# Kernel tuning notes

Hardware: AMD Instinct MI355X
Metric: run time of the kernel (lower is better)

Reference implementation:

```python
import jax, jax.numpy as jnp
import numpy as np
from jax import lax

EPS = 1e-5
TAU = 2.0
THR = 1.0

@jax.custom_vjp
def spike_fn(x):
    # torch.heaviside(x, 1.0): 1 where x >= 0, else 0
    return (x >= 0).astype(x.dtype)

def _spike_fwd(x):
    return spike_fn(x), x

def _spike_bwd(x, g):
    alpha = 4.0
    s = jax.nn.sigmoid(alpha * x)
    return (g * (1.0 - s) * s * alpha,)

spike_fn.defvjp(_spike_fwd, _spike_bwd)

def lif(x):
    # sequential membrane recurrence over dim 0 (time)
    def step(v, xt):
        v = v + (xt - v) / TAU
        s = spike_fn(v - THR)
        v = (1.0 - lax.stop_gradient(s)) * v
        return v, s
    _, spikes = lax.scan(step, jnp.zeros_like(x[0]), x)
    return spikes

def bn(x, p):
    # eval-mode BatchNorm2d; p = [weight, bias, mean, var], each [C]
    w, b, m, v = p
    inv = w / jnp.sqrt(v + EPS)
    return (x - m[None, :, None, None]) * inv[None, :, None, None] + b[None, :, None, None]

def bn_and_pad(x, p):
    # BN then pad 1 pixel on all sides with the BN-of-zero value
    w, b, m, v = p
    y = bn(x, p)
    pad_val = b - m * w / jnp.sqrt(v + EPS)  # [C]
    y = jnp.pad(y, ((0, 0), (0, 0), (1, 1), (1, 1)))
    pv = pad_val[None, :, None]  # broadcasts over batch and spatial
    y = y.at[:, :, 0, :].set(pv)
    y = y.at[:, :, -1, :].set(pv)
    y = y.at[:, :, :, 0].set(pv)
    y = y.at[:, :, :, -1].set(pv)
    return y

def branch(x, w1, dw, pw, bn3):
    # RepConv: 1x1 -> BNAndPad(1) -> depthwise3x3(valid) -> 1x1 -> BN, then outer BN
    C = x.shape[1]
    y = jnp.einsum('oc,bchw->bohw', w1, x)
    y = bn_and_pad(y, bn3[0])
    y = lax.conv_general_dilated(y, dw[:, None, :, :], (1, 1), 'VALID',
                                 dimension_numbers=('NCHW', 'OIHW', 'NCHW'),
                                 feature_group_count=C)
    y = jnp.einsum('oc,bchw->bohw', pw, y)
    y = bn(y, bn3[1])
    y = bn(y, bn3[2])
    return y

def _to_heads(t, B, N, h, d):
    # [B,C,H,W] -> [B,h,N,d]
    return t.reshape(B, h * d, N).transpose(0, 2, 1).reshape(B, N, h, d).transpose(0, 2, 1, 3)

def forward(x, q_w1, q_dw, q_pw, q_bn, k_w1, k_dw, k_pw, k_bn,
            v_w1, v_dw, v_pw, v_bn, p_w1, p_dw, p_pw, p_bn,
            num_heads=8):
    B, C, H, W = x.shape
    N = H * W
    h = num_heads
    d = C // h
    scale = float(d) ** -0.5

    xs = lif(x)
    q = lif(branch(xs, q_w1, q_dw, q_pw, q_bn))
    k = lif(branch(xs, k_w1, k_dw, k_pw, k_bn))
    v = lif(branch(xs, v_w1, v_dw, v_pw, v_bn))

    q = _to_heads(q, B, N, h, d)
    k = _to_heads(k, B, N, h, d)
    v = _to_heads(v, B, N, h, d)

    kv = jnp.einsum('bhnd,bhne->bhde', k, v)          # [B,h,d,d]
    o = jnp.einsum('bhnd,bhde->bhne', q, kv) * scale  # [B,h,N,d]
    o = o.transpose(0, 1, 3, 2).reshape(B, C, N)       # [B,C,N]
    o = lif(o)
    o = o.reshape(B, C, H, W)
    o = branch(o, p_w1, p_dw, p_pw, p_bn)
    return o.reshape(B, C, H, W)

def setup_inputs() -> dict:
    key = jax.random.key(0)
    ks = jax.random.split(key, 20)
    B, C, H, W = 8, 256, 64, 64
    s1 = 1.0 / np.sqrt(C)

    def make_bn(k):
        k1, k2, k3, k4 = jax.random.split(k, 4)
        w = 1.0 + 0.1 * jax.random.normal(k1, (3, C), jnp.float32)
        b = 0.1 * jax.random.normal(k2, (3, C), jnp.float32)
        m = 0.1 * jax.random.normal(k3, (3, C), jnp.float32)
        var = jax.random.uniform(k4, (3, C), jnp.float32, 0.5, 1.5)
        return jnp.stack([w, b, m, var], axis=1)  # [3,4,C]

    inp = {'x': jax.random.normal(ks[0], (B, C, H, W), jnp.float32)}
    for i, p in enumerate(['q', 'k', 'v', 'p']):
        kk = jax.random.split(ks[1 + i], 4)
        inp[p + '_w1'] = jax.random.normal(kk[0], (C, C), jnp.float32) * s1
        inp[p + '_dw'] = jax.random.normal(kk[1], (C, 3, 3), jnp.float32) * 0.3
        inp[p + '_pw'] = jax.random.normal(kk[2], (C, C), jnp.float32) * s1
        inp[p + '_bn'] = make_bn(kk[3])
    return inp

def reference(x, q_w1, q_dw, q_pw, q_bn, k_w1, k_dw, k_pw, k_bn,
              v_w1, v_dw, v_pw, v_bn, p_w1, p_dw, p_pw, p_bn):
    return forward(x, q_w1, q_dw, q_pw, q_bn, k_w1, k_dw, k_pw, k_bn,
                   v_w1, v_dw, v_pw, v_bn, p_w1, p_dw, p_pw, p_bn)
```

## Files before the change

### kernel.cpp

```cpp
#include <hip/hip_runtime.h>
#include <hip/hip_bf16.h>
#include <math.h>

#define T_ 8
#define C_ 256
#define N_ 4096
#define CN_ (C_ * N_)
#define EPSB 1e-5f

typedef unsigned long long u64;
typedef unsigned int u32;
typedef short bf16x8 __attribute__((ext_vector_type(8)));
typedef float f32x4 __attribute__((ext_vector_type(4)));

static __device__ __forceinline__ unsigned short f2bf(float f) {
    __hip_bfloat16 h = __float2bfloat16(f);
    return *(unsigned short*)&h;
}
static __device__ __forceinline__ float bf2f(unsigned short u) {
    u32 x = (u32)u << 16;
    return *(float*)&x;
}


__global__ __launch_bounds__(256) void lif_u8(const float* __restrict__ X,
                                              unsigned char* __restrict__ S) {
    int idx = blockIdx.x * 256 + threadIdx.x;
    float v = 0.f;
#pragma unroll
    for (int t = 0; t < T_; t++) {
        float xt = X[(size_t)t * CN_ + idx];
        v = v + (xt - v) / 2.0f;
        unsigned char s = (v - 1.0f >= 0.f) ? 1 : 0;
        S[(size_t)t * CN_ + idx] = s;
        if (s) v = 0.f;
    }
}

__global__ __launch_bounds__(256) void lif_bp(const float* __restrict__ X,
                                              u64* __restrict__ BP) {
    int idx = blockIdx.x * 256 + threadIdx.x;
    int lane = threadIdx.x & 63;
    float v = 0.f;
#pragma unroll
    for (int t = 0; t < T_; t++) {
        float xt = X[(size_t)t * CN_ + idx];
        v = v + (xt - v) / 2.0f;
        int s = (v - 1.0f >= 0.f) ? 1 : 0;
        u64 mask = __ballot(s);
        if (lane == 0) BP[((size_t)t * CN_ + idx) >> 6] = mask;
        if (s) v = 0.f;
    }
}

struct WPtrs { const float* w[8]; };
__global__ __launch_bounds__(256) void split_w(WPtrs p, unsigned short* __restrict__ out) {
    int mat = blockIdx.y;
    int idx = blockIdx.x * 256 + threadIdx.x;
    int m = idx >> 8, k = idx & 255;
    float w = p.w[mat][idx];
    unsigned short h1 = f2bf(w);
    float f1 = bf2f(h1);
    unsigned short h2 = f2bf(w - f1);
    unsigned short h3 = f2bf(w - f1 - bf2f(h2));
    int lane = ((k >> 3) & 3) * 16 + (m & 15);
    size_t pos = ((size_t)(((m >> 4) * 8 + (k >> 5)) * 64 + lane)) * 8 + (k & 7);
    size_t base = (size_t)mat * 3 * 65536;
    out[base + pos] = h1;
    out[base + 65536 + pos] = h2;
    out[base + 2 * 65536 + pos] = h3;
}

__global__ __launch_bounds__(256) void trans_s(const unsigned char* __restrict__ S,
                                               unsigned short* __restrict__ ST) {
    int t = blockIdx.y;
    int nb = blockIdx.x * 32;
    const unsigned char* St = S + (size_t)t * CN_;
    __shared__ u32 L[32][257];
    int tid = threadIdx.x;
    int nof = (tid & 7) * 4;
    int kbase = tid >> 3;
#pragma unroll
    for (int it = 0; it < 8; it++) {
        int k = kbase + it * 32;
        uchar4 sv = *(const uchar4*)&St[(size_t)k * N_ + nb + nof];
        L[nof + 0][k] = sv.x ? 0x3F80u : 0u;
        L[nof + 1][k] = sv.y ? 0x3F80u : 0u;
        L[nof + 2][k] = sv.z ? 0x3F80u : 0u;
        L[nof + 3][k] = sv.w ? 0x3F80u : 0u;
    }
    __syncthreads();
    int n = tid & 31, k32 = tid >> 5;
    int n16 = (nb + n) >> 4;
    int lrow = n & 15;
    unsigned short* outt = ST + (size_t)t * CN_;
#pragma unroll
    for (int quad = 0; quad < 4; quad++) {
        bf16x8 bs;
#pragma unroll
        for (int j = 0; j < 8; j++)
            bs[j] = (short)(L[n][k32 * 32 + quad * 8 + j] & 0xffffu);
        *(bf16x8*)&outt[((size_t)(n16 * 8 + k32)) * 512 + (quad * 16 + lrow) * 8] = bs;
    }
}

__global__ __launch_bounds__(256) void dw_bn_split(const float* __restrict__ Yin,
                                                   const float* __restrict__ dw,
                                                   const float* __restrict__ bnp,
                                                   unsigned short* __restrict__ BhT,
                                                   unsigned short* __restrict__ BlT) {
    int t = blockIdx.z;
    int y0 = blockIdx.x * 4;
    int cg = blockIdx.y;
    int c0 = cg * 8;
    int tid = threadIdx.x;
    const float* Yt = Yin + (size_t)t * CN_;

    __shared__ float L[8][6][68];
    __shared__ float invs[8], bs_[8], ms_[8], pads_[8];

    if (tid < 8) {
        int c = c0 + tid;
        float w = bnp[c], b = bnp[256 + c], m = bnp[512 + c], var = bnp[768 + c];
        float sq = sqrtf(var + EPSB);
        invs[tid] = w / sq;
        bs_[tid] = b;
        ms_[tid] = m;
        pads_[tid] = b - (m * w) / sq;
    }
    __syncthreads();

    for (int i = tid; i < 8 * 6 * 66; i += 256) {
        int c = i / 396;
        int rem = i - c * 396;
        int row = rem / 66, col = rem - row * 66;
        int gy = y0 - 1 + row, gx = col - 1;
        float val;
        if (gy < 0 || gy > 63 || gx < 0 || gx > 63) val = pads_[c];
        else val = (Yt[(size_t)(c0 + c) * N_ + gy * 64 + gx] - ms_[c]) * invs[c] + bs_[c];
        L[c][row][col] = val;
    }
    __syncthreads();

    int x = tid & 63, ry = tid >> 6;
    int n = (y0 + ry) * 64 + x;

    bf16x8 hi, lo;
#pragma unroll
    for (int j = 0; j < 8; j++) {
        const float* dwc = dw + (c0 + j) * 9;
        float a = 0.f;
#pragma unroll
        for (int dy = 0; dy < 3; dy++)
#pragma unroll
            for (int dx = 0; dx < 3; dx++)
                a += dwc[dy * 3 + dx] * L[j][ry + dy][x + dx];
        unsigned short h = f2bf(a);
        hi[j] = (short)h;
        lo[j] = (short)f2bf(a - bf2f(h));
    }
    size_t pos = ((size_t)((n >> 4) * 8 + (cg >> 2))) * 512 +
                 (size_t)(((cg & 3) * 16 + (n & 15)) * 8);
    *(bf16x8*)&BhT[(size_t)t * CN_ + pos] = hi;
    *(bf16x8*)&BlT[(size_t)t * CN_ + pos] = lo;
}

__global__ __launch_bounds__(256) void gemm_s2(const unsigned short* __restrict__ Wsp,
                                               const unsigned short* __restrict__ ST,
                                               float* __restrict__ Y) {
    int t = blockIdx.z;
    const unsigned short* Bt = ST + (size_t)t * CN_;
    float* Yt = Y + (size_t)t * CN_;
    int bx = blockIdx.x, by = blockIdx.y;
    int tid = threadIdx.x, l = tid & 63, wave = tid >> 6;
    int wm = wave >> 1, wn = wave & 1;
    int lcol = l & 15, quad = l >> 4;

    f32x4 acc[4][4];
#pragma unroll
    for (int i = 0; i < 4; i++)
#pragma unroll
        for (int j = 0; j < 4; j++) acc[i][j] = (f32x4){0.f, 0.f, 0.f, 0.f};

#pragma unroll 2
    for (int k32 = 0; k32 < 8; k32++) {
        bf16x8 bfr[4];
#pragma unroll
        for (int nt = 0; nt < 4; nt++)
            bfr[nt] = *(const bf16x8*)&Bt[((size_t)((bx * 8 + wn * 4 + nt) * 8 + k32)) * 512 + l * 8];
#pragma unroll
        for (int s = 0; s < 3; s++) {
            const unsigned short* Ws = Wsp + (size_t)s * 65536;
#pragma unroll
            for (int mt = 0; mt < 4; mt++) {
                bf16x8 afr = *(const bf16x8*)&Ws[((size_t)((by * 8 + wm * 4 + mt) * 8 + k32)) * 512 + l * 8];
#pragma unroll
                for (int nt = 0; nt < 4; nt++)
                    acc[mt][nt] = __builtin_amdgcn_mfma_f32_16x16x32_bf16(
                        afr, bfr[nt], acc[mt][nt], 0, 0, 0);
            }
        }
    }

    int m0 = by * 128, n0 = bx * 128;
#pragma unroll
    for (int mt = 0; mt < 4; mt++)
#pragma unroll
        for (int i = 0; i < 4; i++) {
            int row = m0 + wm * 64 + mt * 16 + quad * 4 + i;
            float* yr = &Yt[(size_t)row * N_ + n0 + wn * 64 + lcol];
#pragma unroll
            for (int nt = 0; nt < 4; nt++) yr[nt * 16] = acc[mt][nt][i];
        }
}

__global__ __launch_bounds__(256) void gemm_f2(const unsigned short* __restrict__ Wsp,
                                               const unsigned short* __restrict__ BhT,
                                               const unsigned short* __restrict__ BlT,
                                               float* __restrict__ Y,
                                               const float* __restrict__ bnp) {
    int t = blockIdx.z;
    const unsigned short* Bht = BhT + (size_t)t * CN_;
    const unsigned short* Blt = BlT + (size_t)t * CN_;
    float* Yt = Y + (size_t)t * CN_;
    int bx = blockIdx.x, by = blockIdx.y;
    int tid = threadIdx.x, l = tid & 63, wave = tid >> 6;
    int wm = wave >> 1, wn = wave & 1;
    int lcol = l & 15, quad = l >> 4;

    f32x4 acc[4][4];
#pragma unroll
    for (int i = 0; i < 4; i++)
#pragma unroll
        for (int j = 0; j < 4; j++) acc[i][j] = (f32x4){0.f, 0.f, 0.f, 0.f};

#pragma unroll 2
    for (int k32 = 0; k32 < 8; k32++) {
        bf16x8 bh[4], bl[4];
#pragma unroll
        for (int nt = 0; nt < 4; nt++) {
            size_t bpos = ((size_t)((bx * 8 + wn * 4 + nt) * 8 + k32)) * 512 + l * 8;
            bh[nt] = *(const bf16x8*)&Bht[bpos];
            bl[nt] = *(const bf16x8*)&Blt[bpos];
        }
#pragma unroll
        for (int s = 0; s < 3; s++) {
            const unsigned short* Ws = Wsp + (size_t)s * 65536;
#pragma unroll
            for (int mt = 0; mt < 4; mt++) {
                bf16x8 afr = *(const bf16x8*)&Ws[((size_t)((by * 8 + wm * 4 + mt) * 8 + k32)) * 512 + l * 8];
#pragma unroll
                for (int nt = 0; nt < 4; nt++)
                    acc[mt][nt] = __builtin_amdgcn_mfma_f32_16x16x32_bf16(
                        afr, bh[nt], acc[mt][nt], 0, 0, 0);
                if (s < 2) {
#pragma unroll
                    for (int nt = 0; nt < 4; nt++)
                        acc[mt][nt] = __builtin_amdgcn_mfma_f32_16x16x32_bf16(
                            afr, bl[nt], acc[mt][nt], 0, 0, 0);
                }
            }
        }
    }

    int m0 = by * 128, n0 = bx * 128;
#pragma unroll
    for (int mt = 0; mt < 4; mt++)
#pragma unroll
        for (int i = 0; i < 4; i++) {
            int row = m0 + wm * 64 + mt * 16 + quad * 4 + i;
            float i1 = bnp[1024 + row] / sqrtf(bnp[1024 + 768 + row] + EPSB);
            float b1 = bnp[1024 + 256 + row], m1 = bnp[1024 + 512 + row];
            float i2 = bnp[2048 + row] / sqrtf(bnp[2048 + 768 + row] + EPSB);
            float b2 = bnp[2048 + 256 + row], m2 = bnp[2048 + 512 + row];
            float* yr = &Yt[(size_t)row * N_ + n0 + wn * 64 + lcol];
#pragma unroll
            for (int nt = 0; nt < 4; nt++)
                yr[nt * 16] = ((acc[mt][nt][i] - m1) * i1 + b1 - m2) * i2 + b2;
        }
}

__global__ __launch_bounds__(1024) void attn_kv_bp(const u64* __restrict__ Kbp,
                                                   const u64* __restrict__ Vbp,
                                                   float* __restrict__ kvbuf) {
    int th = blockIdx.x;
    int t = th >> 3, h = th & 7;
    const u64* kb = Kbp + ((size_t)t * C_ + h * 32) * 64;
    const u64* vb = Vbp + ((size_t)t * C_ + h * 32) * 64;
    __shared__ u64 ks[32][65];
    __shared__ u64 vs[32][65];
    int tid = threadIdx.x;
    {
        int r = tid >> 5, w2 = (tid & 31) * 2;
        ks[r][w2] = kb[r * 64 + w2];     ks[r][w2 + 1] = kb[r * 64 + w2 + 1];
        vs[r][w2] = vb[r * 64 + w2];     vs[r][w2 + 1] = vb[r * 64 + w2 + 1];
    }
    __syncthreads();
    int d = tid >> 5, e = tid & 31;
    int cnt = 0;
#pragma unroll
    for (int w = 0; w < 64; w++)
        cnt += __popcll(ks[d][w] & vs[e][w]);
    kvbuf[(size_t)th * 1024 + d * 32 + e] = (float)cnt;
}

__global__ __launch_bounds__(256) void attn_o_u8(const unsigned char* __restrict__ q,
                                                 const float* __restrict__ kvbuf,
                                                 float* __restrict__ o) {
    int t = blockIdx.z, h = blockIdx.y;
    int n = blockIdx.x * 1024 + threadIdx.x * 4;
    __shared__ float kvs[1024];
    const float* kv = kvbuf + (size_t)(t * 8 + h) * 1024;
    for (int i = threadIdx.x; i < 1024; i += 256) kvs[i] = kv[i];
    __syncthreads();
    const unsigned char* qb = q + (size_t)t * CN_ + (size_t)h * 32 * N_ + n;
    float* ob = o + (size_t)t * CN_ + (size_t)h * 32 * N_ + n;
    const float scale = 0.17677669529663687f;
#pragma unroll
    for (int eg = 0; eg < 2; eg++) {
        float acc[16][4];
#pragma unroll
        for (int e = 0; e < 16; e++)
#pragma unroll
            for (int j = 0; j < 4; j++) acc[e][j] = 0.f;
        for (int d = 0; d < 32; d++) {
            uchar4 qu = *(const uchar4*)(&qb[(size_t)d * N_]);
            float4 qv = {(float)qu.x, (float)qu.y, (float)qu.z, (float)qu.w};
#pragma unroll
            for (int e = 0; e < 16; e++) {
                float kvv = kvs[d * 32 + eg * 16 + e];
                acc[e][0] += qv.x * kvv;
                acc[e][1] += qv.y * kvv;
                acc[e][2] += qv.z * kvv;
                acc[e][3] += qv.w * kvv;
            }
        }
#pragma unroll
        for (int e = 0; e < 16; e++) {
            float4 ov = {acc[e][0] * scale, acc[e][1] * scale,
                         acc[e][2] * scale, acc[e][3] * scale};
            *(float4*)(&ob[(size_t)(eg * 16 + e) * N_]) = ov;
        }
    }
}

extern "C" void kernel_launch(void* const* d_in, const int* in_sizes, int n_in,
                              void* d_out, int out_size, void* d_ws, size_t ws_size,
                              hipStream_t stream) {
    const float* x = (const float*)d_in[0];
    const float* q_w1 = (const float*)d_in[1];
    const float* q_dw = (const float*)d_in[2];
    const float* q_pw = (const float*)d_in[3];
    const float* q_bn = (const float*)d_in[4];
    const float* k_w1 = (const float*)d_in[5];
    const float* k_dw = (const float*)d_in[6];
    const float* k_pw = (const float*)d_in[7];
    const float* k_bn = (const float*)d_in[8];
    const float* v_w1 = (const float*)d_in[9];
    const float* v_dw = (const float*)d_in[10];
    const float* v_pw = (const float*)d_in[11];
    const float* v_bn = (const float*)d_in[12];
    const float* p_w1 = (const float*)d_in[13];
    const float* p_dw = (const float*)d_in[14];
    const float* p_pw = (const float*)d_in[15];
    const float* p_bn = (const float*)d_in[16];

    const size_t SZ = (size_t)T_ * CN_;
    float* out = (float*)d_out;
    float* S0 = (float*)d_ws;
    float* bufKV = S0 + SZ;
    unsigned char* xs = (unsigned char*)(bufKV + 65536);
    unsigned char* sq = xs + SZ;
    u64* kbp = (u64*)(sq + SZ);
    u64* vbp = kbp + (SZ >> 6);
    unsigned short* wspA = (unsigned short*)(vbp + (SZ >> 6));
    unsigned short* ST = wspA + 8 * 3 * 65536;

    dim3 gLif(CN_ / 256), bLif(256);
    dim3 gGemm(N_ / 128, C_ / 128, T_), bGemm(256);
    dim3 gDwS(16, 32, T_), bDwS(256);
    dim3 gTr(N_ / 32, T_), bTr(256);

    WPtrs wp;
    wp.w[0] = q_w1; wp.w[1] = q_pw; wp.w[2] = k_w1; wp.w[3] = k_pw;
    wp.w[4] = v_w1; wp.w[5] = v_pw; wp.w[6] = p_w1; wp.w[7] = p_pw;
    split_w<<<dim3(256, 8), dim3(256), 0, stream>>>(wp, wspA);
    const size_t WS3 = 3 * 65536;

    unsigned short* outH = (unsigned short*)out;
    unsigned short* outL = outH + SZ;
    unsigned short* s0H = (unsigned short*)S0;
    unsigned short* s0L = s0H + SZ;

    lif_u8<<<gLif, bLif, 0, stream>>>(x, xs);
    trans_s<<<gTr, bTr, 0, stream>>>(xs, ST);

    gemm_s2<<<gGemm, bGemm, 0, stream>>>(wspA + 0 * WS3, ST, S0);
    dw_bn_split<<<gDwS, bDwS, 0, stream>>>(S0, q_dw, q_bn, outH, outL);
    gemm_f2<<<gGemm, bGemm, 0, stream>>>(wspA + 1 * WS3, outH, outL, S0, q_bn);
    lif_u8<<<gLif, bLif, 0, stream>>>(S0, sq);

    gemm_s2<<<gGemm, bGemm, 0, stream>>>(wspA + 2 * WS3, ST, S0);
    dw_bn_split<<<gDwS, bDwS, 0, stream>>>(S0, k_dw, k_bn, outH, outL);
    gemm_f2<<<gGemm, bGemm, 0, stream>>>(wspA + 3 * WS3, outH, outL, S0, k_bn);
    lif_bp<<<gLif, bLif, 0, stream>>>(S0, kbp);

    gemm_s2<<<gGemm, bGemm, 0, stream>>>(wspA + 4 * WS3, ST, S0);
    dw_bn_split<<<gDwS, bDwS, 0, stream>>>(S0, v_dw, v_bn, outH, outL);
    gemm_f2<<<gGemm, bGemm, 0, stream>>>(wspA + 5 * WS3, outH, outL, S0, v_bn);
    lif_bp<<<gLif, bLif, 0, stream>>>(S0, vbp);

    attn_kv_bp<<<dim3(64), dim3(1024), 0, stream>>>(kbp, vbp, bufKV);
    attn_o_u8<<<dim3(4, 8, 8), dim3(256), 0, stream>>>(sq, bufKV, S0);
    lif_u8<<<gLif, bLif, 0, stream>>>(S0, xs);
    trans_s<<<gTr, bTr, 0, stream>>>(xs, ST);

    gemm_s2<<<gGemm, bGemm, 0, stream>>>(wspA + 6 * WS3, ST, out);
    dw_bn_split<<<gDwS, bDwS, 0, stream>>>(out, p_dw, p_bn, s0H, s0L);
    gemm_f2<<<gGemm, bGemm, 0, stream>>>(wspA + 7 * WS3, s0H, s0L, out, p_bn);
}
```

Baseline: 476.9 us.

## Cover full output-channel dimension per block with 1024-thread GEMM tiles

```diff
diff --git a/kernel.cpp b/kernel.cpp
--- a/kernel.cpp
+++ b/kernel.cpp
@@ -165,81 +165,81 @@
     *(bf16x8*)&BlT[(size_t)t * CN_ + pos] = lo;
 }
 
-__global__ __launch_bounds__(256) void gemm_s2(const unsigned short* __restrict__ Wsp,
-                                               const unsigned short* __restrict__ ST,
-                                               float* __restrict__ Y) {
+__global__ __launch_bounds__(1024) void gemm_s2(const unsigned short* __restrict__ Wsp,
+                                                const unsigned short* __restrict__ ST,
+                                                float* __restrict__ Y) {
     int t = blockIdx.z;
     const unsigned short* Bt = ST + (size_t)t * CN_;
     float* Yt = Y + (size_t)t * CN_;
-    int bx = blockIdx.x, by = blockIdx.y;
+    int bx = blockIdx.x;
     int tid = threadIdx.x, l = tid & 63, wave = tid >> 6;
-    int wm = wave >> 1, wn = wave & 1;
+    int wm = wave >> 2, wn = wave & 3;
     int lcol = l & 15, quad = l >> 4;
 
-    f32x4 acc[4][4];
+    f32x4 acc[4][2];
 #pragma unroll
     for (int i = 0; i < 4; i++)
 #pragma unroll
-        for (int j = 0; j < 4; j++) acc[i][j] = (f32x4){0.f, 0.f, 0.f, 0.f};
+        for (int j = 0; j < 2; j++) acc[i][j] = (f32x4){0.f, 0.f, 0.f, 0.f};
 
 #pragma unroll 2
     for (int k32 = 0; k32 < 8; k32++) {
-        bf16x8 bfr[4];
-#pragma unroll
-        for (int nt = 0; nt < 4; nt++)
-            bfr[nt] = *(const bf16x8*)&Bt[((size_t)((bx * 8 + wn * 4 + nt) * 8 + k32)) * 512 + l * 8];
+        bf16x8 bfr[2];
+#pragma unroll
+        for (int nt = 0; nt < 2; nt++)
+            bfr[nt] = *(const bf16x8*)&Bt[((size_t)((bx * 8 + wn * 2 + nt) * 8 + k32)) * 512 + l * 8];
 #pragma unroll
         for (int s = 0; s < 3; s++) {
             const unsigned short* Ws = Wsp + (size_t)s * 65536;
 #pragma unroll
             for (int mt = 0; mt < 4; mt++) {
-                bf16x8 afr = *(const bf16x8*)&Ws[((size_t)((by * 8 + wm * 4 + mt) * 8 + k32)) * 512 + l * 8];
-#pragma unroll
-                for (int nt = 0; nt < 4; nt++)
+                bf16x8 afr = *(const bf16x8*)&Ws[((size_t)((wm * 4 + mt) * 8 + k32)) * 512 + l * 8];
+#pragma unroll
+                for (int nt = 0; nt < 2; nt++)
                     acc[mt][nt] = __builtin_amdgcn_mfma_f32_16x16x32_bf16(
                         afr, bfr[nt], acc[mt][nt], 0, 0, 0);
             }
         }
     }
 
-    int m0 = by * 128, n0 = bx * 128;
+    int n0 = bx * 128 + wn * 32;
 #pragma unroll
     for (int mt = 0; mt < 4; mt++)
 #pragma unroll
         for (int i = 0; i < 4; i++) {
-            int row = m0 + wm * 64 + mt * 16 + quad * 4 + i;
-            float* yr = &Yt[(size_t)row * N_ + n0 + wn * 64 + lcol];
-#pragma unroll
-            for (int nt = 0; nt < 4; nt++) yr[nt * 16] = acc[mt][nt][i];
-        }
-}
-
-__global__ __launch_bounds__(256) void gemm_f2(const unsigned short* __restrict__ Wsp,
-                                               const unsigned short* __restrict__ BhT,
-                                               const unsigned short* __restrict__ BlT,
-                                               float* __restrict__ Y,
-                                               const float* __restrict__ bnp) {
+            int row = wm * 64 + mt * 16 + quad * 4 + i;
+            float* yr = &Yt[(size_t)row * N_ + n0 + lcol];
+            yr[0] = acc[mt][0][i];
+            yr[16] = acc[mt][1][i];
+        }
+}
+
+__global__ __launch_bounds__(1024) void gemm_f2(const unsigned short* __restrict__ Wsp,
+                                                const unsigned short* __restrict__ BhT,
+                                                const unsigned short* __restrict__ BlT,
+                                                float* __restrict__ Y,
+                                                const float* __restrict__ bnp) {
     int t = blockIdx.z;
     const unsigned short* Bht = BhT + (size_t)t * CN_;
     const unsigned short* Blt = BlT + (size_t)t * CN_;
     float* Yt = Y + (size_t)t * CN_;
-    int bx = blockIdx.x, by = blockIdx.y;
+    int bx = blockIdx.x;
     int tid = threadIdx.x, l = tid & 63, wave = tid >> 6;
-    int wm = wave >> 1, wn = wave & 1;
+    int wm = wave >> 2, wn = wave & 3;
     int lcol = l & 15, quad = l >> 4;
 
-    f32x4 acc[4][4];
+    f32x4 acc[4][2];
 #pragma unroll
     for (int i = 0; i < 4; i++)
 #pragma unroll
-        for (int j = 0; j < 4; j++) acc[i][j] = (f32x4){0.f, 0.f, 0.f, 0.f};
+        for (int j = 0; j < 2; j++) acc[i][j] = (f32x4){0.f, 0.f, 0.f, 0.f};
 
 #pragma unroll 2
     for (int k32 = 0; k32 < 8; k32++) {
-        bf16x8 bh[4], bl[4];
-#pragma unroll
-        for (int nt = 0; nt < 4; nt++) {
-            size_t bpos = ((size_t)((bx * 8 + wn * 4 + nt) * 8 + k32)) * 512 + l * 8;
+        bf16x8 bh[2], bl[2];
+#pragma unroll
+        for (int nt = 0; nt < 2; nt++) {
+            size_t bpos = ((size_t)((bx * 8 + wn * 2 + nt) * 8 + k32)) * 512 + l * 8;
             bh[nt] = *(const bf16x8*)&Bht[bpos];
             bl[nt] = *(const bf16x8*)&Blt[bpos];
         }
@@ -248,14 +248,14 @@
             const unsigned short* Ws = Wsp + (size_t)s * 65536;
 #pragma unroll
             for (int mt = 0; mt < 4; mt++) {
-                bf16x8 afr = *(const bf16x8*)&Ws[((size_t)((by * 8 + wm * 4 + mt) * 8 + k32)) * 512 + l * 8];
-#pragma unroll
-                for (int nt = 0; nt < 4; nt++)
+                bf16x8 afr = *(const bf16x8*)&Ws[((size_t)((wm * 4 + mt) * 8 + k32)) * 512 + l * 8];
+#pragma unroll
+                for (int nt = 0; nt < 2; nt++)
                     acc[mt][nt] = __builtin_amdgcn_mfma_f32_16x16x32_bf16(
                         afr, bh[nt], acc[mt][nt], 0, 0, 0);
                 if (s < 2) {
 #pragma unroll
-                    for (int nt = 0; nt < 4; nt++)
+                    for (int nt = 0; nt < 2; nt++)
                         acc[mt][nt] = __builtin_amdgcn_mfma_f32_16x16x32_bf16(
                             afr, bl[nt], acc[mt][nt], 0, 0, 0);
                 }
@@ -263,20 +263,19 @@
         }
     }
 
-    int m0 = by * 128, n0 = bx * 128;
+    int n0 = bx * 128 + wn * 32;
 #pragma unroll
     for (int mt = 0; mt < 4; mt++)
 #pragma unroll
         for (int i = 0; i < 4; i++) {
-            int row = m0 + wm * 64 + mt * 16 + quad * 4 + i;
+            int row = wm * 64 + mt * 16 + quad * 4 + i;
             float i1 = bnp[1024 + row] / sqrtf(bnp[1024 + 768 + row] + EPSB);
             float b1 = bnp[1024 + 256 + row], m1 = bnp[1024 + 512 + row];
             float i2 = bnp[2048 + row] / sqrtf(bnp[2048 + 768 + row] + EPSB);
             float b2 = bnp[2048 + 256 + row], m2 = bnp[2048 + 512 + row];
-            float* yr = &Yt[(size_t)row * N_ + n0 + wn * 64 + lcol];
-#pragma unroll
-            for (int nt = 0; nt < 4; nt++)
-                yr[nt * 16] = ((acc[mt][nt][i] - m1) * i1 + b1 - m2) * i2 + b2;
+            float* yr = &Yt[(size_t)row * N_ + n0 + lcol];
+            yr[0] = ((acc[mt][0][i] - m1) * i1 + b1 - m2) * i2 + b2;
+            yr[16] = ((acc[mt][1][i] - m1) * i1 + b1 - m2) * i2 + b2;
         }
 }
 
@@ -377,7 +376,7 @@
     unsigned short* ST = wspA + 8 * 3 * 65536;
 
     dim3 gLif(CN_ / 256), bLif(256);
-    dim3 gGemm(N_ / 128, C_ / 128, T_), bGemm(256);
+    dim3 gGemm(N_ / 128, 1, T_), bGemm(1024);
     dim3 gDwS(16, 32, T_), bDwS(256);
     dim3 gTr(N_ / 32, T_), bTr(256);
 
```

Result: slower. 507.1 us (+6.3%).

## Batch Q/K/V branch kernels into single launches over a branch grid dimension

Applied to the files above, without the earlier changes.

```diff
diff --git a/kernel.cpp b/kernel.cpp
--- a/kernel.cpp
+++ b/kernel.cpp
@@ -37,18 +37,30 @@
     }
 }
 
-__global__ __launch_bounds__(256) void lif_bp(const float* __restrict__ X,
-                                              u64* __restrict__ BP) {
+struct LArgs {
+    const float* F[3];
+    unsigned char* sq;
+    u64* kbp;
+    u64* vbp;
+};
+__global__ __launch_bounds__(256) void lif3(LArgs a) {
+    int br = blockIdx.y;
     int idx = blockIdx.x * 256 + threadIdx.x;
+    const float* X = a.F[br];
     int lane = threadIdx.x & 63;
+    u64* BP = (br == 1) ? a.kbp : a.vbp;
     float v = 0.f;
 #pragma unroll
     for (int t = 0; t < T_; t++) {
         float xt = X[(size_t)t * CN_ + idx];
         v = v + (xt - v) / 2.0f;
         int s = (v - 1.0f >= 0.f) ? 1 : 0;
-        u64 mask = __ballot(s);
-        if (lane == 0) BP[((size_t)t * CN_ + idx) >> 6] = mask;
+        if (br == 0) {
+            a.sq[(size_t)t * CN_ + idx] = (unsigned char)s;
+        } else {
+            u64 mask = __ballot(s);
+            if (lane == 0) BP[((size_t)t * CN_ + idx) >> 6] = mask;
+        }
         if (s) v = 0.f;
     }
 }
@@ -104,18 +116,13 @@
     }
 }
 
-__global__ __launch_bounds__(256) void dw_bn_split(const float* __restrict__ Yin,
-                                                   const float* __restrict__ dw,
-                                                   const float* __restrict__ bnp,
-                                                   unsigned short* __restrict__ BhT,
-                                                   unsigned short* __restrict__ BlT) {
-    int t = blockIdx.z;
-    int y0 = blockIdx.x * 4;
-    int cg = blockIdx.y;
+static __device__ __forceinline__ void dw_body(const float* __restrict__ Yt,
+                                               const float* __restrict__ dw,
+                                               const float* __restrict__ bnp,
+                                               unsigned short* __restrict__ Bh,
+                                               unsigned short* __restrict__ Bl,
+                                               int y0, int cg, int tid) {
     int c0 = cg * 8;
-    int tid = threadIdx.x;
-    const float* Yt = Yin + (size_t)t * CN_;
-
     __shared__ float L[8][6][68];
     __shared__ float invs[8], bs_[8], ms_[8], pads_[8];
 
@@ -161,18 +168,40 @@
     }
     size_t pos = ((size_t)((n >> 4) * 8 + (cg >> 2))) * 512 +
                  (size_t)(((cg & 3) * 16 + (n & 15)) * 8);
-    *(bf16x8*)&BhT[(size_t)t * CN_ + pos] = hi;
-    *(bf16x8*)&BlT[(size_t)t * CN_ + pos] = lo;
-}
-
-__global__ __launch_bounds__(256) void gemm_s2(const unsigned short* __restrict__ Wsp,
-                                               const unsigned short* __restrict__ ST,
-                                               float* __restrict__ Y) {
+    *(bf16x8*)&Bh[pos] = hi;
+    *(bf16x8*)&Bl[pos] = lo;
+}
+
+__global__ __launch_bounds__(256) void dw_bn_split(const float* __restrict__ Yin,
+                                                   const float* __restrict__ dw,
+                                                   const float* __restrict__ bnp,
+                                                   unsigned short* __restrict__ BhT,
+                                                   unsigned short* __restrict__ BlT) {
     int t = blockIdx.z;
-    const unsigned short* Bt = ST + (size_t)t * CN_;
-    float* Yt = Y + (size_t)t * CN_;
-    int bx = blockIdx.x, by = blockIdx.y;
-    int tid = threadIdx.x, l = tid & 63, wave = tid >> 6;
+    dw_body(Yin + (size_t)t * CN_, dw, bnp,
+            BhT + (size_t)t * CN_, BlT + (size_t)t * CN_,
+            blockIdx.x * 4, blockIdx.y, threadIdx.x);
+}
+
+struct DArgs {
+    const float* F[3];
+    const float* dw[3];
+    const float* bn[3];
+    unsigned short* Ph[3];
+    unsigned short* Pl[3];
+};
+__global__ __launch_bounds__(256) void dw3(DArgs a) {
+    int br = blockIdx.z >> 3, t = blockIdx.z & 7;
+    dw_body(a.F[br] + (size_t)t * CN_, a.dw[br], a.bn[br],
+            a.Ph[br] + (size_t)t * CN_, a.Pl[br] + (size_t)t * CN_,
+            blockIdx.x * 4, blockIdx.y, threadIdx.x);
+}
+
+static __device__ __forceinline__ void gemm_s_core(const unsigned short* __restrict__ Wsp,
+                                                   const unsigned short* __restrict__ Bt,
+                                                   float* __restrict__ Yt,
+                                                   int bx, int by, int tid) {
+    int l = tid & 63, wave = tid >> 6;
     int wm = wave >> 1, wn = wave & 1;
     int lcol = l & 15, quad = l >> 4;
 
@@ -214,17 +243,13 @@
         }
 }
 
-__global__ __launch_bounds__(256) void gemm_f2(const unsigned short* __restrict__ Wsp,
-                                               const unsigned short* __restrict__ BhT,
-                                               const unsigned short* __restrict__ BlT,
-                                               float* __restrict__ Y,
-                                               const float* __restrict__ bnp) {
-    int t = blockIdx.z;
-    const unsigned short* Bht = BhT + (size_t)t * CN_;
-    const unsigned short* Blt = BlT + (size_t)t * CN_;
-    float* Yt = Y + (size_t)t * CN_;
-    int bx = blockIdx.x, by = blockIdx.y;
-    int tid = threadIdx.x, l = tid & 63, wave = tid >> 6;
+static __device__ __forceinline__ void gemm_f_core(const unsigned short* __restrict__ Wsp,
+                                                   const unsigned short* __restrict__ Bht,
+                                                   const unsigned short* __restrict__ Blt,
+                                                   float* __restrict__ Yt,
+                                                   const float* __restrict__ bnp,
+                                                   int bx, int by, int tid) {
+    int l = tid & 63, wave = tid >> 6;
     int wm = wave >> 1, wn = wave & 1;
     int lcol = l & 15, quad = l >> 4;
 
@@ -278,6 +303,44 @@
             for (int nt = 0; nt < 4; nt++)
                 yr[nt * 16] = ((acc[mt][nt][i] - m1) * i1 + b1 - m2) * i2 + b2;
         }
+}
+
+__global__ __launch_bounds__(256) void gemm_s2(const unsigned short* __restrict__ Wsp,
+                                               const unsigned short* __restrict__ ST,
+                                               float* __restrict__ Y) {
+    int t = blockIdx.z;
+    gemm_s_core(Wsp, ST + (size_t)t * CN_, Y + (size_t)t * CN_,
+                blockIdx.x, blockIdx.y, threadIdx.x);
+}
+__global__ __launch_bounds__(256) void gemm_f2(const unsigned short* __restrict__ Wsp,
+                                               const unsigned short* __restrict__ BhT,
+                                               const unsigned short* __restrict__ BlT,
+                                               float* __restrict__ Y,
+                                               const float* __restrict__ bnp) {
+    int t = blockIdx.z;
+    gemm_f_core(Wsp, BhT + (size_t)t * CN_, BlT + (size_t)t * CN_,
+                Y + (size_t)t * CN_, bnp, blockIdx.x, blockIdx.y, threadIdx.x);
+}
+
+struct GSArgs { const unsigned short* W[3]; const unsigned short* ST; float* F[3]; };
+__global__ __launch_bounds__(256) void gemm_s3(GSArgs a) {
+    int t = blockIdx.z;
+    int br = blockIdx.y >> 1, byl = blockIdx.y & 1;
+    gemm_s_core(a.W[br], a.ST + (size_t)t * CN_, a.F[br] + (size_t)t * CN_,
+                blockIdx.x, byl, threadIdx.x);
+}
+struct GFArgs {
+    const unsigned short* W[3];
+    const unsigned short* Ph[3];
+    const unsigned short* Pl[3];
+    float* F[3];
+    const float* bn[3];
+};
+__global__ __launch_bounds__(256) void gemm_f3(GFArgs a) {
+    int t = blockIdx.z;
+    int br = blockIdx.y >> 1, byl = blockIdx.y & 1;
+    gemm_f_core(a.W[br], a.Ph[br] + (size_t)t * CN_, a.Pl[br] + (size_t)t * CN_,
+                a.F[br] + (size_t)t * CN_, a.bn[br], blockIdx.x, byl, threadIdx.x);
 }
 
 __global__ __launch_bounds__(1024) void attn_kv_bp(const u64* __restrict__ Kbp,
@@ -367,8 +430,13 @@
 
     const size_t SZ = (size_t)T_ * CN_;
     float* out = (float*)d_out;
-    float* S0 = (float*)d_ws;
-    float* bufKV = S0 + SZ;
+    float* F0 = (float*)d_ws;
+    float* F1 = F0 + SZ;
+    float* F2 = F1 + SZ;
+    float* P0 = F2 + SZ;
+    float* P1 = P0 + SZ;
+    float* P2 = P1 + SZ;
+    float* bufKV = P2 + SZ;
     unsigned char* xs = (unsigned char*)(bufKV + 65536);
     unsigned char* sq = xs + SZ;
     u64* kbp = (u64*)(sq + SZ);
@@ -376,9 +444,11 @@
     unsigned short* wspA = (unsigned short*)(vbp + (SZ >> 6));
     unsigned short* ST = wspA + 8 * 3 * 65536;
 
+    unsigned short* P0h = (unsigned short*)P0; unsigned short* P0l = P0h + SZ;
+    unsigned short* P1h = (unsigned short*)P1; unsigned short* P1l = P1h + SZ;
+    unsigned short* P2h = (unsigned short*)P2; unsigned short* P2l = P2h + SZ;
+
     dim3 gLif(CN_ / 256), bLif(256);
-    dim3 gGemm(N_ / 128, C_ / 128, T_), bGemm(256);
-    dim3 gDwS(16, 32, T_), bDwS(256);
     dim3 gTr(N_ / 32, T_), bTr(256);
 
     WPtrs wp;
@@ -387,35 +457,41 @@
     split_w<<<dim3(256, 8), dim3(256), 0, stream>>>(wp, wspA);
     const size_t WS3 = 3 * 65536;
 
-    unsigned short* outH = (unsigned short*)out;
-    unsigned short* outL = outH + SZ;
-    unsigned short* s0H = (unsigned short*)S0;
-    unsigned short* s0L = s0H + SZ;
-
     lif_u8<<<gLif, bLif, 0, stream>>>(x, xs);
     trans_s<<<gTr, bTr, 0, stream>>>(xs, ST);
 
-    gemm_s2<<<gGemm, bGemm, 0, stream>>>(wspA + 0 * WS3, ST, S0);
-    dw_bn_split<<<gDwS, bDwS, 0, stream>>>(S0, q_dw, q_bn, outH, outL);
-    gemm_f2<<<gGemm, bGemm, 0, stream>>>(wspA + 1 * WS3, outH, outL, S0, q_bn);
-    lif_u8<<<gLif, bLif, 0, stream>>>(S0, sq);
-
-    gemm_s2<<<gGemm, bGemm, 0, stream>>>(wspA + 2 * WS3, ST, S0);
-    dw_bn_split<<<gDwS, bDwS, 0, stream>>>(S0, k_dw, k_bn, outH, outL);
-    gemm_f2<<<gGemm, bGemm, 0, stream>>>(wspA + 3 * WS3, outH, outL, S0, k_bn);
-    lif_bp<<<gLif, bLif, 0, stream>>>(S0, kbp);
-
-    gemm_s2<<<gGemm, bGemm, 0, stream>>>(wspA + 4 * WS3, ST, S0);
-    dw_bn_split<<<gDwS, bDwS, 0, stream>>>(S0, v_dw, v_bn, outH, outL);
-    gemm_f2<<<gGemm, bGemm, 0, stream>>>(wspA + 5 * WS3, outH, outL, S0, v_bn);
-    lif_bp<<<gLif, bLif, 0, stream>>>(S0, vbp);
+    GSArgs gs;
+    gs.W[0] = wspA + 0 * WS3; gs.W[1] = wspA + 2 * WS3; gs.W[2] = wspA + 4 * WS3;
+    gs.ST = ST; gs.F[0] = F0; gs.F[1] = F1; gs.F[2] = F2;
+    gemm_s3<<<dim3(N_ / 128, 6, T_), dim3(256), 0, stream>>>(gs);
+
+    DArgs da;
+    da.F[0] = F0; da.F[1] = F1; da.F[2] = F2;
+    da.dw[0] = q_dw; da.dw[1] = k_dw; da.dw[2] = v_dw;
+    da.bn[0] = q_bn; da.bn[1] = k_bn; da.bn[2] = v_bn;
+    da.Ph[0] = P0h; da.Ph[1] = P1h; da.Ph[2] = P2h;
+    da.Pl[0] = P0l; da.Pl[1] = P1l; da.Pl[2] = P2l;
+    dw3<<<dim3(16, 32, 3 * T_), dim3(256), 0, stream>>>(da);
+
+    GFArgs gf;
+    gf.W[0] = wspA + 1 * WS3; gf.W[1] = wspA + 3 * WS3; gf.W[2] = wspA + 5 * WS3;
+    gf.Ph[0] = P0h; gf.Ph[1] = P1h; gf.Ph[2] = P2h;
+    gf.Pl[0] = P0l; gf.Pl[1] = P1l; gf.Pl[2] = P2l;
+    gf.F[0] = F0; gf.F[1] = F1; gf.F[2] = F2;
+    gf.bn[0] = q_bn; gf.bn[1] = k_bn; gf.bn[2] = v_bn;
+    gemm_f3<<<dim3(N_ / 128, 6, T_), dim3(256), 0, stream>>>(gf);
+
+    LArgs la;
+    la.F[0] = F0; la.F[1] = F1; la.F[2] = F2;
+    la.sq = sq; la.kbp = kbp; la.vbp = vbp;
+    lif3<<<dim3(CN_ / 256, 3), dim3(256), 0, stream>>>(la);
 
     attn_kv_bp<<<dim3(64), dim3(1024), 0, stream>>>(kbp, vbp, bufKV);
-    attn_o_u8<<<dim3(4, 8, 8), dim3(256), 0, stream>>>(sq, bufKV, S0);
-    lif_u8<<<gLif, bLif, 0, stream>>>(S0, xs);
+    attn_o_u8<<<dim3(4, 8, 8), dim3(256), 0, stream>>>(sq, bufKV, F0);
+    lif_u8<<<gLif, bLif, 0, stream>>>(F0, xs);
     trans_s<<<gTr, bTr, 0, stream>>>(xs, ST);
 
-    gemm_s2<<<gGemm, bGemm, 0, stream>>>(wspA + 6 * WS3, ST, out);
-    dw_bn_split<<<gDwS, bDwS, 0, stream>>>(out, p_dw, p_bn, s0H, s0L);
-    gemm_f2<<<gGemm, bGemm, 0, stream>>>(wspA + 7 * WS3, s0H, s0L, out, p_bn);
-}
+    gemm_s2<<<dim3(N_ / 128, C_ / 128, T_), dim3(256), 0, stream>>>(wspA + 6 * WS3, ST, out);
+    dw_bn_split<<<dim3(16, 32, T_), dim3(256), 0, stream>>>(out, p_dw, p_bn, P0h, P0l);
+    gemm_f2<<<dim3(N_ / 128, C_ / 128, T_), dim3(256), 0, stream>>>(wspA + 7 * WS3, P0h, P0l, out, p_bn);
+}
```

New measurement: 442.7 us. 7.2% less time.
